# Performance work log

Measured on AMD Instinct MI355X. Metric: run time of the kernel, lower is better.

## Reference

```python
import jax, jax.numpy as jnp
import numpy as np

B, S, E = 2, 2048, 1024          # batch, seq, emb_size
H, D = 16, 64                     # heads, head_dim
NE, K = 8, 2                      # num_experts, top_k


def setup_inputs() -> dict:
    key = jax.random.key(0)
    ks = jax.random.split(key, 12)
    w = lambda k, shape: jax.random.normal(k, shape, jnp.float32) * 0.02
    return {
        "x": jax.random.normal(ks[0], (B, S, E), jnp.float32),
        "q_w": w(ks[1], (E, E)), "q_b": jnp.zeros((E,), jnp.float32),
        "k_w": w(ks[2], (E, E)), "k_b": jnp.zeros((E,), jnp.float32),
        "v_w": w(ks[3], (E, E)), "v_b": jnp.zeros((E,), jnp.float32),
        "gate_w": w(ks[4], (NE, E)), "gate_b": jnp.zeros((NE,), jnp.float32),
        "expert_w": w(ks[5], (NE, E, E)), "expert_b": jnp.zeros((NE, E), jnp.float32),
        "ffn_w": w(ks[6], (E, E)), "ffn_b": jnp.zeros((E,), jnp.float32),
    }


def _rope_cos_sin(seq_len, dim):
    inv_freq = 1.0 / (10000.0 ** (jnp.arange(0, dim, 2, dtype=jnp.float32) / dim))
    freqs = jnp.outer(jnp.arange(seq_len, dtype=jnp.float32), inv_freq)  # [S, D/2]
    emb = jnp.concatenate([freqs, freqs], axis=-1)                        # [S, D]
    return jnp.cos(emb), jnp.sin(emb)


def _rotate_half(x):
    x1, x2 = jnp.split(x, 2, axis=-1)
    return jnp.concatenate([-x2, x1], axis=-1)


def reference(x, q_w, q_b, k_w, k_b, v_w, v_b, gate_w, gate_b, expert_w, expert_b, ffn_w, ffn_b):
    b, s, _ = x.shape
    q = (x @ q_w.T + q_b).reshape(b, s, H, D)
    k = (x @ k_w.T + k_b).reshape(b, s, H, D)
    v = (x @ v_w.T + v_b).reshape(b, s, H, D)

    cos, sin = _rope_cos_sin(s, D)          # [S, D]
    cos = cos[None, :, None, :]
    sin = sin[None, :, None, :]
    q = q * cos + _rotate_half(q) * sin
    k = k * cos + _rotate_half(k) * sin

    # full (memory-efficient-style) attention, scale 1/sqrt(D)
    scores = jnp.einsum('bqhd,bkhd->bhqk', q, k) / jnp.sqrt(jnp.float32(D))
    attn = jax.nn.softmax(scores, axis=-1)
    attn_out = jnp.einsum('bhqk,bkhd->bqhd', attn, v).reshape(b, s, E)

    # MoE: dense-compute all experts, gather top-k, weighted combine
    gates = jax.nn.softmax(attn_out @ gate_w.T + gate_b, axis=-1)        # [B,S,NE]
    top_gates, top_idx = jax.lax.top_k(gates, K)                          # [B,S,K]
    # Linear per expert: y = x W^T + b,  expert_w: [NE, out, in]
    expert_outputs = jnp.einsum('bsi,noi->bsno', attn_out, expert_w) + expert_b  # [B,S,NE,E]
    sel = jnp.take_along_axis(expert_outputs, top_idx[..., None], axis=2)        # [B,S,K,E]
    moe_out = jnp.einsum('bsk,bskh->bsh', top_gates, sel)                        # [B,S,E]

    # dropout is identity at inference; ffn + residual
    return moe_out @ ffn_w.T + ffn_b + x
```

## Files before the change

### kernel.cpp

```cpp
#include <hip/hip_runtime.h>
#include <hip/hip_bf16.h>

#define B_ 2
#define S_ 2048
#define E_ 1024
#define H_ 16
#define D_ 64
#define NE_ 8
#define TOKENS (B_*S_)
#define QSCALE 0.18033688011112043f

typedef __attribute__((ext_vector_type(8))) short bf16x8;
typedef __attribute__((ext_vector_type(4))) float f32x4;
typedef unsigned short u16;
typedef unsigned int u32;

#if __has_builtin(__builtin_amdgcn_exp2f)
#define EXP2(x) __builtin_amdgcn_exp2f(x)
#else
#define EXP2(x) exp2f(x)
#endif

__device__ __forceinline__ u16 f2bf(float f) {
    u32 u = __float_as_uint(f);
    u32 r = u + 0x7fffu + ((u >> 16) & 1u);
    return (u16)(r >> 16);
}
__device__ __forceinline__ float bf2f(u16 h) {
    return __uint_as_float(((u32)h) << 16);
}
__device__ __forceinline__ void gl2lds16(const void* g, void* l) {
    __builtin_amdgcn_global_load_lds(
        (__attribute__((address_space(1))) void*)(g),
        (__attribute__((address_space(3))) void*)(l), 16, 0, 0);
}
#define MFMA16(a,b,c) __builtin_amdgcn_mfma_f32_16x16x32_bf16(a,b,c,0,0,0)

__global__ void cvt_all_k(
    const float* __restrict__ x,  const float* __restrict__ qw,
    const float* __restrict__ kw, const float* __restrict__ vw,
    const float* __restrict__ fw, const float* __restrict__ ew,
    u16* __restrict__ xh,  u16* __restrict__ qwh, u16* __restrict__ kwh,
    u16* __restrict__ vwh, u16* __restrict__ fwh, u16* __restrict__ ewh,
    float2* __restrict__ tab)
{
    const int blk = blockIdx.x;
    if (blk >= 16384) {
        const int idx = (blk - 16384) * 256 + threadIdx.x;
        const int s = idx >> 5, d1 = idx & 31;
        const float inv = exp2f(-(float)d1 * 0.41524101186091903f);
        float sn, cs;
        sincosf((float)s * inv, &sn, &cs);
        tab[idx] = make_float2(cs, sn);
        return;
    }
    const float* s; u16* d; int off;
    if (blk < 4096)      { s = x;  d = xh;  off = blk; }
    else if (blk < 5120) { s = qw; d = qwh; off = blk - 4096; }
    else if (blk < 6144) { s = kw; d = kwh; off = blk - 5120; }
    else if (blk < 7168) { s = vw; d = vwh; off = blk - 6144; }
    else if (blk < 8192) { s = fw; d = fwh; off = blk - 7168; }
    else                 { s = ew; d = ewh; off = blk - 8192; }
    const size_t i = (size_t)off * 256 + threadIdx.x;
    const float4 v = *(const float4*)(s + i * 4);
    ushort4 H = {f2bf(v.x), f2bf(v.y), f2bf(v.z), f2bf(v.w)};
    *(ushort4*)(d + i * 4) = H;
}

__global__ __launch_bounds__(256,2) void gemm_qkv(
    const u16* __restrict__ Ah,
    const u16* __restrict__ qwh, const u16* __restrict__ kwh,
    const u16* __restrict__ vwh,
    const float* __restrict__ q_b, const float* __restrict__ k_b,
    const float* __restrict__ v_b,
    const float2* __restrict__ tab,
    u16* __restrict__ Qhb, u16* __restrict__ Khb, u16* __restrict__ Vtb)
{
    __shared__ __align__(16) u16 sA[128*32], sB[128*32];
    const int z = blockIdx.z;
    const u16* Bh = (z == 0) ? qwh : (z == 1) ? kwh : vwh;
    const float* bias = (z == 0) ? q_b : (z == 1) ? k_b : v_b;
    const int t = threadIdx.x;
    const int m0 = blockIdx.y * 128, n0 = blockIdx.x * 128;
    const int lane = t & 63, w = t >> 6;
    const int wm = w >> 1, wn = w & 1;
    const int lr = lane & 15, qd = lane >> 4;
    f32x4 acc[4][4] = {};
    const size_t gA = (size_t)(m0 + (t >> 2)) * E_ + (t & 3) * 8;
    const size_t gB = (size_t)(n0 + (t >> 2)) * E_ + (t & 3) * 8;
    for (int k0 = 0; k0 < E_; k0 += 32) {
        #pragma unroll
        for (int is = 0; is < 2; is++) {
            const int ldo = (is * 256 + (t & 192)) * 16;
            const size_t ro = (size_t)is * 64 * E_;
            gl2lds16(Ah + gA + ro + k0, (char*)sA + ldo);
            gl2lds16(Bh + gB + ro + k0, (char*)sB + ldo);
        }
        __syncthreads();
        bf16x8 af[4], bfr[4];
        #pragma unroll
        for (int i = 0; i < 4; i++) {
            af[i]  = *(const bf16x8*)&sA[(wm*64 + i*16 + lr)*32 + qd*8];
            bfr[i] = *(const bf16x8*)&sB[(wn*64 + i*16 + lr)*32 + qd*8];
        }
        #pragma unroll
        for (int i = 0; i < 4; i++)
            #pragma unroll
            for (int j = 0; j < 4; j++)
                acc[i][j] = MFMA16(af[i], bfr[j], acc[i][j]);
        __syncthreads();
    }
    const int head = (n0 + wn * 64) >> 6;
    if (z < 2) {
        u16* Oh = (z == 0) ? Qhb : Khb;
        const float osc = (z == 0) ? QSCALE : 1.0f;
        #pragma unroll
        for (int j = 0; j < 2; j++) {
            const int d1 = j * 16 + lr;
            const float b1 = bias[head * 64 + d1];
            const float b2 = bias[head * 64 + d1 + 32];
            #pragma unroll
            for (int i = 0; i < 4; i++) {
                #pragma unroll
                for (int r = 0; r < 4; r++) {
                    const int tok = m0 + wm*64 + i*16 + qd*4 + r;
                    const int bb = tok >> 11, ss = tok & (S_ - 1);
                    const float2 t2 = tab[ss * 32 + d1];
                    const float q1 = acc[i][j][r]   + b1;
                    const float q2 = acc[i][j+2][r] + b2;
                    const size_t o = (((size_t)bb * H_ + head) * S_ + ss) * 64 + d1;
                    Oh[o]    = f2bf((q1 * t2.x - q2 * t2.y) * osc);
                    Oh[o+32] = f2bf((q2 * t2.x + q1 * t2.y) * osc);
                }
            }
        }
    } else {
        #pragma unroll
        for (int j = 0; j < 4; j++) {
            const int d = j * 16 + lr;
            const float bv = bias[head * 64 + d];
            #pragma unroll
            for (int i = 0; i < 4; i++)
                #pragma unroll
                for (int r = 0; r < 4; r++) {
                    const int tok = m0 + wm*64 + i*16 + qd*4 + r;
                    const int bb = tok >> 11, ss = tok & (S_ - 1);
                    Vtb[(((size_t)bb * H_ + head) * 64 + d) * S_ + ss] = f2bf(acc[i][j][r] + bv);
                }
        }
    }
}

__global__ __launch_bounds__(256,4) void attn_kernel(
    const u16* __restrict__ Q, const u16* __restrict__ K,
    const u16* __restrict__ Vt,
    float* __restrict__ Opart, float* __restrict__ lpart)
{
    __shared__ __align__(16) u16 sK[2][64*64];
    __shared__ __align__(16) u16 sV[2][64*64];
    __shared__ __align__(16) u16 sP[4][672];
    const int t = threadIdx.x, lane = t & 63, w = t >> 6;
    const int lr = lane & 15, qd = lane >> 4;
    const int lin = blockIdx.x + (blockIdx.y << 4) + (blockIdx.z << 8);
    const int wg  = ((lin & 7) << 7) + (lin >> 3);
    const int q0 = (wg & 15) << 7;
    const int h  = (wg >> 4) & 15;
    const int zc = wg >> 8;
    const int b = zc & 1, sc = zc >> 1;
    const size_t bhS = ((size_t)b * H_ + h) * S_;
    const size_t bhD = ((size_t)b * H_ + h) * 64;
    bf16x8 qf[2][2];
    #pragma unroll
    for (int p = 0; p < 2; p++) {
        const size_t qa = (bhS + q0 + p*64 + w*16 + lr) * 64 + qd * 8;
        qf[p][0] = *(const bf16x8*)&Q[qa];
        qf[p][1] = *(const bf16x8*)&Q[qa + 32];
    }
    bf16x8 vOnes;
    #pragma unroll
    for (int i = 0; i < 8; i++) vOnes[i] = (short)0x3F80;
    f32x4 O[2][4] = {};
    f32x4 Ol[2] = {};

    const int CH0 = w*4 + qd, CH1 = (4 + w)*4 + qd;
    const int sbs0 = CH0 >> 3, doff0 = ((CH0 >> 2) & 1)*32 + (CH0 & 3)*8;
    const int sbs1 = CH1 >> 3, doff1 = ((CH1 >> 2) & 1)*32 + (CH1 & 3)*8;
    auto stage = [&](int bp, int j0) {
        gl2lds16(&K [(bhS + j0 + sbs0*16 + lr)*64 + doff0], (char*)sK[bp] + w*1024);
        gl2lds16(&Vt[(bhD + sbs0*16 + lr)*S_ + j0 + doff0], (char*)sV[bp] + w*1024);
        gl2lds16(&K [(bhS + j0 + sbs1*16 + lr)*64 + doff1], (char*)sK[bp] + (4+w)*1024);
        gl2lds16(&Vt[(bhD + sbs1*16 + lr)*S_ + j0 + doff1], (char*)sV[bp] + (4+w)*1024);
    };

    const int jbeg = sc * 1024;
    stage(0, jbeg);
    for (int jt = 0; jt < 16; ++jt) {
        const int cur = jt & 1;
        asm volatile("s_waitcnt vmcnt(0) lgkmcnt(0)" ::: "memory");
        __builtin_amdgcn_sched_barrier(0);
        __builtin_amdgcn_s_barrier();
        __builtin_amdgcn_sched_barrier(0);
        if (jt + 1 < 16) stage(cur ^ 1, jbeg + (jt + 1) * 64);
        f32x4 Sv[2][4];
        __builtin_amdgcn_s_setprio(1);
        #pragma unroll
        for (int sb = 0; sb < 4; sb++) {
            bf16x8 k0 = *(const bf16x8*)&sK[cur][(sb*8 + qd)*128 + lr*8];
            bf16x8 k1 = *(const bf16x8*)&sK[cur][(sb*8 + 4 + qd)*128 + lr*8];
            f32x4 a0 = {}, a1 = {};
            a0 = MFMA16(k0, qf[0][0], a0);
            a0 = MFMA16(k1, qf[0][1], a0);
            a1 = MFMA16(k0, qf[1][0], a1);
            a1 = MFMA16(k1, qf[1][1], a1);
            Sv[0][sb] = a0;
            Sv[1][sb] = a1;
        }
        __builtin_amdgcn_s_setprio(0);
        uint2 pk[2][4];
        #pragma unroll
        for (int p = 0; p < 2; p++) {
            #pragma unroll
            for (int sb = 0; sb < 4; sb++) {
                const float pv0 = EXP2(Sv[p][sb][0]);
                const float pv1 = EXP2(Sv[p][sb][1]);
                const float pv2 = EXP2(Sv[p][sb][2]);
                const float pv3 = EXP2(Sv[p][sb][3]);
                pk[p][sb].x = __builtin_amdgcn_perm(__float_as_uint(pv1),
                                                    __float_as_uint(pv0), 0x07060302u);
                pk[p][sb].y = __builtin_amdgcn_perm(__float_as_uint(pv3),
                                                    __float_as_uint(pv2), 0x07060302u);
            }
        }
        bf16x8 vv[8];
        #pragma unroll
        for (int ds = 0; ds < 4; ds++) {
            vv[2*ds]   = *(const bf16x8*)&sV[cur][(ds*8 + qd)*128 + lr*8];
            vv[2*ds+1] = *(const bf16x8*)&sV[cur][(ds*8 + 4 + qd)*128 + lr*8];
        }
        #pragma unroll
        for (int p = 0; p < 2; p++) {
            #pragma unroll
            for (int sb = 0; sb < 4; sb++)
                *(uint2*)&sP[w][lr*40 + sb*16 + qd*4] = pk[p][sb];
            bf16x8 p0 = *(const bf16x8*)&sP[w][lr*40 + qd*8];
            bf16x8 p1 = *(const bf16x8*)&sP[w][lr*40 + 32 + qd*8];
            __builtin_amdgcn_s_setprio(1);
            #pragma unroll
            for (int ds = 0; ds < 4; ds++) {
                O[p][ds] = MFMA16(p0, vv[2*ds],   O[p][ds]);
                O[p][ds] = MFMA16(p1, vv[2*ds+1], O[p][ds]);
            }
            Ol[p] = MFMA16(p0, vOnes, Ol[p]);
            Ol[p] = MFMA16(p1, vOnes, Ol[p]);
            __builtin_amdgcn_s_setprio(0);
        }
    }
    float* Op = Opart + (size_t)sc * TOKENS * E_;
    float* lp = lpart + (size_t)sc * TOKENS * H_;
    if (lr == 0) {
        #pragma unroll
        for (int p = 0; p < 2; p++)
            #pragma unroll
            for (int r = 0; r < 4; r++)
                lp[(size_t)(b*S_ + q0 + p*64 + w*16 + qd*4 + r) * H_ + h] = Ol[p][r];
    }
    #pragma unroll
    for (int p = 0; p < 2; p++) {
        const int qb = q0 + p*64 + w*16 + qd*4;
        #pragma unroll
        for (int ds = 0; ds < 4; ds++)
            #pragma unroll
            for (int r = 0; r < 4; r++)
                Op[(size_t)(b*S_ + qb + r) * E_ + h*64 + ds*16 + lr] = O[p][ds][r];
    }
}

__global__ __launch_bounds__(256) void combine_gate(
    const float* __restrict__ Opart, const float* __restrict__ lpart,
    const float* __restrict__ gate_w, const float* __restrict__ gate_b,
    u16* __restrict__ attn_bf, float* __restrict__ gval, int* __restrict__ eidx)
{
    __shared__ float red[4][NE_];
    __shared__ float lg8[NE_];
    const int tok = blockIdx.x;
    const int t = threadIdx.x;
    const int d4 = t * 4;
    const int h = d4 >> 6;
    const float l = lpart[(size_t)tok*H_ + h] + lpart[(size_t)(TOKENS + tok)*H_ + h];
    const float inv = 1.f / l;
    const float4 o1 = *(const float4*)&Opart[(size_t)tok*E_ + d4];
    const float4 o2 = *(const float4*)&Opart[(size_t)(TOKENS + tok)*E_ + d4];
    float v[4] = {(o1.x+o2.x)*inv, (o1.y+o2.y)*inv, (o1.z+o2.z)*inv, (o1.w+o2.w)*inv};
    ushort4 H4 = {f2bf(v[0]), f2bf(v[1]), f2bf(v[2]), f2bf(v[3])};
    *(ushort4*)&attn_bf[(size_t)tok*E_ + d4] = H4;
    float pe[NE_];
    #pragma unroll
    for (int e = 0; e < NE_; e++) {
        const float4 g = *(const float4*)&gate_w[e*E_ + d4];
        pe[e] = v[0]*g.x + v[1]*g.y + v[2]*g.z + v[3]*g.w;
    }
    #pragma unroll
    for (int e = 0; e < NE_; e++) {
        #pragma unroll
        for (int off = 32; off >= 1; off >>= 1)
            pe[e] += __shfl_xor(pe[e], off, 64);
    }
    const int w = t >> 6;
    if ((t & 63) == 0) {
        #pragma unroll
        for (int e = 0; e < NE_; e++) red[w][e] = pe[e];
    }
    __syncthreads();
    if (t < NE_)
        lg8[t] = red[0][t] + red[1][t] + red[2][t] + red[3][t] + gate_b[t];
    __syncthreads();
    if (t == 0) {
        float lg[NE_];
        #pragma unroll
        for (int e = 0; e < NE_; e++) lg[e] = lg8[e];
        float m = lg[0];
        #pragma unroll
        for (int e = 1; e < NE_; e++) m = fmaxf(m, lg[e]);
        float ex[NE_], ssum = 0.f;
        #pragma unroll
        for (int e = 0; e < NE_; e++) { ex[e] = __expf(lg[e]-m); ssum += ex[e]; }
        const float invs = 1.f / ssum;
        int i0 = 0;
        #pragma unroll
        for (int e = 1; e < NE_; e++) if (lg[e] > lg[i0]) i0 = e;
        int i1 = (i0 == 0) ? 1 : 0;
        #pragma unroll
        for (int e = 0; e < NE_; e++) if (e != i0 && lg[e] > lg[i1]) i1 = e;
        eidx[tok*2]     = i0;
        gval[tok*2]     = ex[i0]*invs;
        eidx[tok*2 + 1] = i1;
        gval[tok*2 + 1] = ex[i1]*invs;
    }
}

__global__ __launch_bounds__(256) void build_lists_kernel(
    const int* __restrict__ eidx, int* __restrict__ list, int* __restrict__ counts)
{
    __shared__ int lcnt[NE_], lbase[NE_];
    const int t = threadIdx.x;
    if (t < NE_) lcnt[t] = 0;
    __syncthreads();
    const int ent = blockIdx.x * 512 + t * 2;
    const int e0 = eidx[ent], e1 = eidx[ent + 1];
    const int p0 = atomicAdd(&lcnt[e0], 1);
    const int p1 = atomicAdd(&lcnt[e1], 1);
    __syncthreads();
    if (t < NE_) lbase[t] = atomicAdd(&counts[t], lcnt[t]);
    __syncthreads();
    list[e0 * TOKENS + lbase[e0] + p0] = ent;
    list[e1 * TOKENS + lbase[e1] + p1] = ent + 1;
}

__global__ __launch_bounds__(256,2) void gemm_expert(
    const u16* __restrict__ Abf, const u16* __restrict__ ewh,
    const float* __restrict__ eb, const int* __restrict__ list,
    const int* __restrict__ counts, const float* __restrict__ gval,
    u16* __restrict__ sel)
{
    const int e = blockIdx.z;
    const int cnt = counts[e];
    const int m0 = blockIdx.y * 128;
    if (m0 >= cnt) return;
    __shared__ __align__(16) u16 sA[128*32], sB[128*32];
    __shared__ int sEnt[128];
    const int t = threadIdx.x;
    if (t < 128) sEnt[t] = (m0 + t < cnt) ? list[e * TOKENS + m0 + t] : -1;
    __syncthreads();
    const int n0 = blockIdx.x * 128;
    const int lane = t & 63, w = t >> 6;
    const int wm = w >> 1, wn = w & 1;
    const int lr = lane & 15, qd = lane >> 4;
    const int e0 = sEnt[t >> 2], e1 = sEnt[64 + (t >> 2)];
    const u16* ga0 = Abf + (size_t)(e0 < 0 ? 0 : (e0 >> 1)) * E_ + (t & 3) * 8;
    const u16* ga1 = Abf + (size_t)(e1 < 0 ? 0 : (e1 >> 1)) * E_ + (t & 3) * 8;
    const u16* gb0 = ewh + (size_t)e * E_ * E_ + (size_t)(n0 + (t >> 2)) * E_ + (t & 3) * 8;
    const u16* gb1 = gb0 + 64 * E_;
    f32x4 acc[4][4] = {};
    for (int k0 = 0; k0 < E_; k0 += 32) {
        {
            const int l0 = (t & 192) * 16;
            const int l1 = (256 + (t & 192)) * 16;
            gl2lds16(ga0 + k0, (char*)sA + l0);
            gl2lds16(ga1 + k0, (char*)sA + l1);
            gl2lds16(gb0 + k0, (char*)sB + l0);
            gl2lds16(gb1 + k0, (char*)sB + l1);
        }
        __syncthreads();
        bf16x8 af[4], bfr[4];
        #pragma unroll
        for (int i = 0; i < 4; i++) {
            af[i]  = *(const bf16x8*)&sA[(wm*64 + i*16 + lr)*32 + qd*8];
            bfr[i] = *(const bf16x8*)&sB[(wn*64 + i*16 + lr)*32 + qd*8];
        }
        #pragma unroll
        for (int i = 0; i < 4; i++)
            #pragma unroll
            for (int j = 0; j < 4; j++)
                acc[i][j] = MFMA16(af[i], bfr[j], acc[i][j]);
        __syncthreads();
    }
    #pragma unroll
    for (int i = 0; i < 4; i++)
        #pragma unroll
        for (int r = 0; r < 4; r++) {
            const int local = wm*64 + i*16 + qd*4 + r;
            const int ent = sEnt[local];
            if (ent < 0) continue;
            const float g = gval[ent];
            #pragma unroll
            for (int j = 0; j < 4; j++) {
                const int col = n0 + wn*64 + j*16 + lr;
                sel[(size_t)ent * E_ + col] = f2bf((acc[i][j][r] + eb[e * E_ + col]) * g);
            }
        }
}

__global__ void combine_kernel(const u16* __restrict__ sel, u16* __restrict__ moe)
{
    const int g = blockIdx.x * 256 + threadIdx.x;
    const int tok = g >> 8;
    const int c = (g & 255) * 4;
    const u16* a = sel + (size_t)tok * 2048 + c;
    float o[4];
    #pragma unroll
    for (int j = 0; j < 4; j++) o[j] = bf2f(a[j]) + bf2f(a[1024 + j]);
    ushort4 R = {f2bf(o[0]), f2bf(o[1]), f2bf(o[2]), f2bf(o[3])};
    *(ushort4*)(moe + (size_t)tok * E_ + c) = R;
}

__global__ __launch_bounds__(256,2) void gemm_ffn(
    const u16* __restrict__ Ah, const u16* __restrict__ Bh,
    const float* __restrict__ bias, const float* __restrict__ res,
    float* __restrict__ C)
{
    __shared__ __align__(16) u16 sA[128*32], sB[128*32];
    const int t = threadIdx.x;
    const int m0 = blockIdx.y * 128, n0 = blockIdx.x * 128;
    const int lane = t & 63, w = t >> 6;
    const int wm = w >> 1, wn = w & 1;
    const int lr = lane & 15, qd = lane >> 4;
    f32x4 acc[4][4] = {};
    const size_t gA = (size_t)(m0 + (t >> 2)) * E_ + (t & 3) * 8;
    const size_t gB = (size_t)(n0 + (t >> 2)) * E_ + (t & 3) * 8;
    for (int k0 = 0; k0 < E_; k0 += 32) {
        #pragma unroll
        for (int is = 0; is < 2; is++) {
            const int ldo = (is * 256 + (t & 192)) * 16;
            const size_t ro = (size_t)is * 64 * E_;
            gl2lds16(Ah + gA + ro + k0, (char*)sA + ldo);
            gl2lds16(Bh + gB + ro + k0, (char*)sB + ldo);
        }
        __syncthreads();
        bf16x8 af[4], bfr[4];
        #pragma unroll
        for (int i = 0; i < 4; i++) {
            af[i]  = *(const bf16x8*)&sA[(wm*64 + i*16 + lr)*32 + qd*8];
            bfr[i] = *(const bf16x8*)&sB[(wn*64 + i*16 + lr)*32 + qd*8];
        }
        #pragma unroll
        for (int i = 0; i < 4; i++)
            #pragma unroll
            for (int j = 0; j < 4; j++)
                acc[i][j] = MFMA16(af[i], bfr[j], acc[i][j]);
        __syncthreads();
    }
    #pragma unroll
    for (int i = 0; i < 4; i++)
        #pragma unroll
        for (int r = 0; r < 4; r++) {
            const int tok = m0 + wm*64 + i*16 + qd*4 + r;
            #pragma unroll
            for (int j = 0; j < 4; j++) {
                const int col = n0 + wn*64 + j*16 + lr;
                C[(size_t)tok * E_ + col] = acc[i][j][r] + bias[col] + res[(size_t)tok * E_ + col];
            }
        }
}

extern "C" void kernel_launch(void* const* d_in, const int* in_sizes, int n_in,
                              void* d_out, int out_size, void* d_ws, size_t ws_size,
                              hipStream_t stream) {
    const float* x      = (const float*)d_in[0];
    const float* q_w    = (const float*)d_in[1];
    const float* q_b    = (const float*)d_in[2];
    const float* k_w    = (const float*)d_in[3];
    const float* k_b    = (const float*)d_in[4];
    const float* v_w    = (const float*)d_in[5];
    const float* v_b    = (const float*)d_in[6];
    const float* gate_w = (const float*)d_in[7];
    const float* gate_b = (const float*)d_in[8];
    const float* ew     = (const float*)d_in[9];
    const float* eb     = (const float*)d_in[10];
    const float* ffn_w  = (const float*)d_in[11];
    const float* ffn_b  = (const float*)d_in[12];
    float* out = (float*)d_out;

    char* p = (char*)d_ws;
    auto alloc = [&](size_t bytes) { char* r = p; p += (bytes + 255) & ~(size_t)255; return r; };
    u16* xh   = (u16*)alloc((size_t)TOKENS*E_*2);
    u16* qwh  = (u16*)alloc((size_t)E_*E_*2);
    u16* kwh  = (u16*)alloc((size_t)E_*E_*2);
    u16* vwh  = (u16*)alloc((size_t)E_*E_*2);
    u16* fwh  = (u16*)alloc((size_t)E_*E_*2);
    u16* ewh  = (u16*)alloc((size_t)NE_*E_*E_*2);
    u16* Qhb  = (u16*)alloc((size_t)TOKENS*E_*2);
    u16* Khb  = (u16*)alloc((size_t)TOKENS*E_*2);
    u16* Vtb  = (u16*)alloc((size_t)TOKENS*E_*2);
    u16* abf  = (u16*)alloc((size_t)TOKENS*E_*2);
    float* Opart = (float*)alloc((size_t)2*TOKENS*E_*4);
    float* lpart = (float*)alloc((size_t)2*TOKENS*H_*4);
    u16* selb = (u16*)alloc((size_t)2*TOKENS*E_*2);
    u16* moeb = (u16*)alloc((size_t)TOKENS*E_*2);
    float2* rtab = (float2*)alloc((size_t)S_*32*8);
    float* gvl = (float*)alloc((size_t)2*TOKENS*4);
    int*   eix = (int*)alloc((size_t)2*TOKENS*4);
    int*   lst = (int*)alloc((size_t)NE_*TOKENS*4);
    int*   cnt = (int*)alloc(256);

    hipMemsetAsync(cnt, 0, 256, stream);

    cvt_all_k<<<16640, 256, 0, stream>>>(x, q_w, k_w, v_w, ffn_w, ew,
                                         xh, qwh, kwh, vwh, fwh, ewh, rtab);

    gemm_qkv<<<dim3(8,32,3), 256, 0, stream>>>(xh, qwh, kwh, vwh,
                                               q_b, k_b, v_b, rtab,
                                               Qhb, Khb, Vtb);

    attn_kernel<<<dim3(16,16,4), 256, 0, stream>>>(Qhb, Khb, Vtb, Opart, lpart);

    combine_gate<<<TOKENS, 256, 0, stream>>>(Opart, lpart, gate_w, gate_b,
                                             abf, gvl, eix);
    build_lists_kernel<<<TOKENS/256, 256, 0, stream>>>(eix, lst, cnt);
    gemm_expert<<<dim3(8,32,8), 256, 0, stream>>>(abf, ewh, eb, lst, cnt, gvl, selb);
    combine_kernel<<<4096, 256, 0, stream>>>(selb, moeb);
    gemm_ffn<<<dim3(8,32), 256, 0, stream>>>(moeb, fwh, ffn_b, x, out);
}
```

Before: 289.7 us.

## Switch attention kernel to 32x32x16 MFMA with register-only P transpose via permlane32_swap

Rewrites the attention inner loop to use 32x32x16 bf16 MFMA tiles, so each wave handles 32 query rows instead of two 16-row groups. The P matrix is no longer transposed through the per-wave LDS scratch buffer; it is rearranged in registers with v_permlane32_swap. The K/V staging layout and output indexing change to match. This cuts LDS traffic and instruction count per tile, but depends on the fragment layout and swap mapping being exactly right.

New measurement: 297.9 us. +2.8%, slower.

```diff
diff --git a/kernel.cpp b/kernel.cpp
--- a/kernel.cpp
+++ b/kernel.cpp
@@ -12,8 +12,10 @@
 
 typedef __attribute__((ext_vector_type(8))) short bf16x8;
 typedef __attribute__((ext_vector_type(4))) float f32x4;
+typedef __attribute__((ext_vector_type(16))) float f32x16;
 typedef unsigned short u16;
 typedef unsigned int u32;
+typedef __attribute__((ext_vector_type(4))) u32 u32x4;
 
 #if __has_builtin(__builtin_amdgcn_exp2f)
 #define EXP2(x) __builtin_amdgcn_exp2f(x)
@@ -35,6 +37,7 @@
         (__attribute__((address_space(3))) void*)(l), 16, 0, 0);
 }
 #define MFMA16(a,b,c) __builtin_amdgcn_mfma_f32_16x16x32_bf16(a,b,c,0,0,0)
+#define MFMA32(a,b,c) __builtin_amdgcn_mfma_f32_32x32x16_bf16(a,b,c,0,0,0)
 
 __global__ void cvt_all_k(
     const float* __restrict__ x,  const float* __restrict__ qw,
@@ -158,9 +161,8 @@
 {
     __shared__ __align__(16) u16 sK[2][64*64];
     __shared__ __align__(16) u16 sV[2][64*64];
-    __shared__ __align__(16) u16 sP[4][672];
     const int t = threadIdx.x, lane = t & 63, w = t >> 6;
-    const int lr = lane & 15, qd = lane >> 4;
+    const int lq = lane & 31, hi = lane >> 5;
     const int lin = blockIdx.x + (blockIdx.y << 4) + (blockIdx.z << 8);
     const int wg  = ((lin & 7) << 7) + (lin >> 3);
     const int q0 = (wg & 15) << 7;
@@ -169,27 +171,24 @@
     const int b = zc & 1, sc = zc >> 1;
     const size_t bhS = ((size_t)b * H_ + h) * S_;
     const size_t bhD = ((size_t)b * H_ + h) * 64;
-    bf16x8 qf[2][2];
-    #pragma unroll
-    for (int p = 0; p < 2; p++) {
-        const size_t qa = (bhS + q0 + p*64 + w*16 + lr) * 64 + qd * 8;
-        qf[p][0] = *(const bf16x8*)&Q[qa];
-        qf[p][1] = *(const bf16x8*)&Q[qa + 32];
-    }
+    bf16x8 qf[4];
+    #pragma unroll
+    for (int ks = 0; ks < 4; ks++)
+        qf[ks] = *(const bf16x8*)&Q[(bhS + q0 + w*32 + lq) * 64 + ks*16 + hi*8];
     bf16x8 vOnes;
     #pragma unroll
     for (int i = 0; i < 8; i++) vOnes[i] = (short)0x3F80;
-    f32x4 O[2][4] = {};
-    f32x4 Ol[2] = {};
-
-    const int CH0 = w*4 + qd, CH1 = (4 + w)*4 + qd;
-    const int sbs0 = CH0 >> 3, doff0 = ((CH0 >> 2) & 1)*32 + (CH0 & 3)*8;
-    const int sbs1 = CH1 >> 3, doff1 = ((CH1 >> 2) & 1)*32 + (CH1 & 3)*8;
+    f32x16 O[2] = {};
+    f32x16 Ol = {};
+
+    const int f0 = w*2, f1 = w*2 + 1;
+    const int kR0 = (f0>>2)*32 + lq, kC0 = (f0&3)*16 + hi*8;
+    const int kR1 = (f1>>2)*32 + lq, kC1 = (f1&3)*16 + hi*8;
     auto stage = [&](int bp, int j0) {
-        gl2lds16(&K [(bhS + j0 + sbs0*16 + lr)*64 + doff0], (char*)sK[bp] + w*1024);
-        gl2lds16(&Vt[(bhD + sbs0*16 + lr)*S_ + j0 + doff0], (char*)sV[bp] + w*1024);
-        gl2lds16(&K [(bhS + j0 + sbs1*16 + lr)*64 + doff1], (char*)sK[bp] + (4+w)*1024);
-        gl2lds16(&Vt[(bhD + sbs1*16 + lr)*S_ + j0 + doff1], (char*)sV[bp] + (4+w)*1024);
+        gl2lds16(&K [(bhS + j0 + kR0)*64 + kC0], (char*)sK[bp] + f0*1024);
+        gl2lds16(&K [(bhS + j0 + kR1)*64 + kC1], (char*)sK[bp] + f1*1024);
+        gl2lds16(&Vt[(bhD + kR0)*S_ + j0 + kC0], (char*)sV[bp] + f0*1024);
+        gl2lds16(&Vt[(bhD + kR1)*S_ + j0 + kC1], (char*)sV[bp] + f1*1024);
     };
 
     const int jbeg = sc * 1024;
@@ -201,78 +200,59 @@
         __builtin_amdgcn_s_barrier();
         __builtin_amdgcn_sched_barrier(0);
         if (jt + 1 < 16) stage(cur ^ 1, jbeg + (jt + 1) * 64);
-        f32x4 Sv[2][4];
-        __builtin_amdgcn_s_setprio(1);
-        #pragma unroll
-        for (int sb = 0; sb < 4; sb++) {
-            bf16x8 k0 = *(const bf16x8*)&sK[cur][(sb*8 + qd)*128 + lr*8];
-            bf16x8 k1 = *(const bf16x8*)&sK[cur][(sb*8 + 4 + qd)*128 + lr*8];
-            f32x4 a0 = {}, a1 = {};
-            a0 = MFMA16(k0, qf[0][0], a0);
-            a0 = MFMA16(k1, qf[0][1], a0);
-            a1 = MFMA16(k0, qf[1][0], a1);
-            a1 = MFMA16(k1, qf[1][1], a1);
-            Sv[0][sb] = a0;
-            Sv[1][sb] = a1;
-        }
-        __builtin_amdgcn_s_setprio(0);
-        uint2 pk[2][4];
-        #pragma unroll
-        for (int p = 0; p < 2; p++) {
-            #pragma unroll
-            for (int sb = 0; sb < 4; sb++) {
-                const float pv0 = EXP2(Sv[p][sb][0]);
-                const float pv1 = EXP2(Sv[p][sb][1]);
-                const float pv2 = EXP2(Sv[p][sb][2]);
-                const float pv3 = EXP2(Sv[p][sb][3]);
-                pk[p][sb].x = __builtin_amdgcn_perm(__float_as_uint(pv1),
-                                                    __float_as_uint(pv0), 0x07060302u);
-                pk[p][sb].y = __builtin_amdgcn_perm(__float_as_uint(pv3),
-                                                    __float_as_uint(pv2), 0x07060302u);
+        u32 pk[16];
+        #pragma unroll
+        for (int kb = 0; kb < 2; kb++) {
+            f32x16 Sv = {};
+            __builtin_amdgcn_s_setprio(1);
+            #pragma unroll
+            for (int ks = 0; ks < 4; ks++) {
+                const bf16x8 kf = *(const bf16x8*)&sK[cur][(kb*4 + ks)*512 + lane*8];
+                Sv = MFMA32(kf, qf[ks], Sv);
             }
-        }
-        bf16x8 vv[8];
-        #pragma unroll
-        for (int ds = 0; ds < 4; ds++) {
-            vv[2*ds]   = *(const bf16x8*)&sV[cur][(ds*8 + qd)*128 + lr*8];
-            vv[2*ds+1] = *(const bf16x8*)&sV[cur][(ds*8 + 4 + qd)*128 + lr*8];
-        }
-        #pragma unroll
-        for (int p = 0; p < 2; p++) {
-            #pragma unroll
-            for (int sb = 0; sb < 4; sb++)
-                *(uint2*)&sP[w][lr*40 + sb*16 + qd*4] = pk[p][sb];
-            bf16x8 p0 = *(const bf16x8*)&sP[w][lr*40 + qd*8];
-            bf16x8 p1 = *(const bf16x8*)&sP[w][lr*40 + 32 + qd*8];
+            __builtin_amdgcn_s_setprio(0);
+            #pragma unroll
+            for (int j = 0; j < 8; j++) {
+                const float e0 = EXP2(Sv[2*j]);
+                const float e1 = EXP2(Sv[2*j+1]);
+                pk[kb*8 + j] = __builtin_amdgcn_perm(__float_as_uint(e1),
+                                                     __float_as_uint(e0), 0x07060302u);
+            }
+        }
+        #pragma unroll
+        for (int ks = 0; ks < 4; ks++) {
+            const int base = (ks >> 1)*8 + (ks & 1)*4;
+            u32 a0 = pk[base],     b0 = pk[base + 2];
+            u32 a1 = pk[base + 1], b1 = pk[base + 3];
+            asm("v_permlane32_swap_b32 %0, %1" : "+v"(a0), "+v"(b0));
+            asm("v_permlane32_swap_b32 %0, %1" : "+v"(a1), "+v"(b1));
+            u32x4 fv; fv.x = a0; fv.y = a1; fv.z = b0; fv.w = b1;
+            const bf16x8 pa = __builtin_bit_cast(bf16x8, fv);
+            const bf16x8 vf0 = *(const bf16x8*)&sV[cur][(0*4 + ks)*512 + lane*8];
+            const bf16x8 vf1 = *(const bf16x8*)&sV[cur][(1*4 + ks)*512 + lane*8];
             __builtin_amdgcn_s_setprio(1);
-            #pragma unroll
-            for (int ds = 0; ds < 4; ds++) {
-                O[p][ds] = MFMA16(p0, vv[2*ds],   O[p][ds]);
-                O[p][ds] = MFMA16(p1, vv[2*ds+1], O[p][ds]);
-            }
-            Ol[p] = MFMA16(p0, vOnes, Ol[p]);
-            Ol[p] = MFMA16(p1, vOnes, Ol[p]);
+            O[0] = MFMA32(pa, vf0, O[0]);
+            O[1] = MFMA32(pa, vf1, O[1]);
+            Ol   = MFMA32(pa, vOnes, Ol);
             __builtin_amdgcn_s_setprio(0);
         }
     }
     float* Op = Opart + (size_t)sc * TOKENS * E_;
     float* lp = lpart + (size_t)sc * TOKENS * H_;
-    if (lr == 0) {
-        #pragma unroll
-        for (int p = 0; p < 2; p++)
-            #pragma unroll
-            for (int r = 0; r < 4; r++)
-                lp[(size_t)(b*S_ + q0 + p*64 + w*16 + qd*4 + r) * H_ + h] = Ol[p][r];
-    }
-    #pragma unroll
-    for (int p = 0; p < 2; p++) {
-        const int qb = q0 + p*64 + w*16 + qd*4;
-        #pragma unroll
-        for (int ds = 0; ds < 4; ds++)
-            #pragma unroll
-            for (int r = 0; r < 4; r++)
-                Op[(size_t)(b*S_ + qb + r) * E_ + h*64 + ds*16 + lr] = O[p][ds][r];
-    }
+    if (lq == 0) {
+        #pragma unroll
+        for (int r = 0; r < 16; r++) {
+            const int qr = (r & 3) + 8*(r >> 2) + 4*hi;
+            lp[(size_t)(b*S_ + q0 + w*32 + qr) * H_ + h] = Ol[r];
+        }
+    }
+    #pragma unroll
+    for (int cb = 0; cb < 2; cb++)
+        #pragma unroll
+        for (int r = 0; r < 16; r++) {
+            const int qr = (r & 3) + 8*(r >> 2) + 4*hi;
+            Op[(size_t)(b*S_ + q0 + w*32 + qr) * E_ + h*64 + cb*32 + lq] = O[cb][r];
+        }
 }
 
 __global__ __launch_bounds__(256) void combine_gate(
```
